# Kernel tuning notes

Hardware: AMD Instinct MI355X
Metric: run time of the kernel (lower is better)

## Reference

```python
import jax, jax.numpy as jnp
import numpy as np

N = 50000      # nodes
E = 400000     # directed edges
F_IN = 128     # input features
H0, C0 = 4, 64     # layer0: 4 heads x 64, concat -> 256
H1, C1 = 1, 256    # layer1: 1 head x 256, mean/concat -> 256
NCLS = 10
SLOPE = 0.2    # PyG GATConv leaky_relu negative_slope


def setup_inputs() -> dict:
    key = jax.random.key(0)
    ks = jax.random.split(key, 20)
    g = lambda k, shape, fan_in: jax.random.normal(k, shape, jnp.float32) * (1.0 / np.sqrt(fan_in))
    x = jax.random.normal(ks[0], (N, F_IN), jnp.float32)
    edge_index = jax.random.randint(ks[1], (2, E), 0, N)
    return {
        "x": x,
        "edge_index": edge_index,
        # GATConv layer 0: 128 -> 4 heads x 64, concat
        "W0": g(ks[2], (F_IN, H0 * C0), F_IN),
        "a_src0": g(ks[3], (H0, C0), C0),
        "a_dst0": g(ks[4], (H0, C0), C0),
        "b0": jnp.zeros((H0 * C0,), jnp.float32),
        # GATConv layer 1: 256 -> 1 head x 256, averaged
        "W1": g(ks[5], (H0 * C0, H1 * C1), H0 * C0),
        "a_src1": g(ks[6], (H1, C1), C1),
        "a_dst1": g(ks[7], (H1, C1), C1),
        "b1": jnp.zeros((C1,), jnp.float32),
        # MLP head 256 -> 512 -> 1024 -> NCLS
        "lw1": g(ks[8], (256, 512), 256), "lb1": jnp.zeros((512,), jnp.float32),
        "lw2": g(ks[9], (512, 1024), 512), "lb2": jnp.zeros((1024,), jnp.float32),
        "lw3": g(ks[10], (1024, NCLS), 1024), "lb3": jnp.zeros((NCLS,), jnp.float32),
    }


def _gat_conv(x, src, dst, valid, W, a_src, a_dst, b, heads, ch, concat):
    """PyG GATConv (eval mode, dropout=0): gather -> edge attention ->
    softmax over incoming edges per target -> scatter-sum aggregate."""
    n = x.shape[0]
    h = (x @ W).reshape(n, heads, ch)                      # [N,H,C]
    alpha_src = jnp.sum(h * a_src[None], axis=-1)          # [N,H]
    alpha_dst = jnp.sum(h * a_dst[None], axis=-1)          # [N,H]
    e = jax.nn.leaky_relu(alpha_src[src] + alpha_dst[dst], SLOPE)  # [Etot,H]
    e = jnp.where(valid[:, None], e, -1e9)                 # removed self-loops
    emax = jax.lax.stop_gradient(jax.ops.segment_max(e, dst, num_segments=n))
    w = jnp.exp(e - emax[dst]) * valid[:, None].astype(e.dtype)
    denom = jax.ops.segment_sum(w, dst, num_segments=n)    # [N,H] (>0: self-loops)
    w = w / denom[dst]
    out = jax.ops.segment_sum(h[src] * w[..., None], dst, num_segments=n)  # [N,H,C]
    out = out.reshape(n, heads * ch) if concat else out.mean(axis=1)
    return out + b


def reference(x, edge_index, W0, a_src0, a_dst0, b0, W1, a_src1, a_dst1, b1,
              lw1, lb1, lw2, lb2, lw3, lb3):
    n = x.shape[0]
    s0, d0 = edge_index[0], edge_index[1]
    loop = jnp.arange(n, dtype=s0.dtype)
    src = jnp.concatenate([s0, loop])
    dst = jnp.concatenate([d0, loop])
    valid = jnp.concatenate([s0 != d0, jnp.ones((n,), bool)])  # remove+add self-loops
    h = jax.nn.relu(_gat_conv(x, src, dst, valid, W0, a_src0, a_dst0, b0, H0, C0, True))
    h = jax.nn.relu(_gat_conv(h, src, dst, valid, W1, a_src1, a_dst1, b1, H1, C1, False))
    h = jax.nn.relu(h @ lw1 + lb1)
    h = jax.nn.relu(h @ lw2 + lb2)
    h = jax.nn.relu(h @ lw3 + lb3)
    return jax.nn.softmax(h, axis=1)
```

## Files before the change

kernel.cpp:

```cpp
#include <hip/hip_runtime.h>
#include <cstdint>
#include <cstddef>

#define F_IN   128
#define SLOPE  0.2f

typedef unsigned short u16;
typedef __attribute__((ext_vector_type(8))) short     bf16x8;
typedef __attribute__((ext_vector_type(8))) unsigned short u16x8;
typedef __attribute__((ext_vector_type(4))) unsigned short u16x4;
typedef __attribute__((ext_vector_type(4))) float     f32x4;

__device__ __forceinline__ u16 f2bf(float f) {
    unsigned u = __float_as_uint(f);
    unsigned r = u + 0x7FFFu + ((u >> 16) & 1u);
    return (u16)(r >> 16);
}
__device__ __forceinline__ float bf2f(u16 h) {
    return __uint_as_float(((unsigned)h) << 16);
}

__device__ __forceinline__ float lrelu(float v) { return v >= 0.f ? v : SLOPE * v; }

__global__ void alphas0_k(const float* __restrict__ h0, const float* __restrict__ a_src,
                          const float* __restrict__ a_dst, float* __restrict__ asrc,
                          float* __restrict__ adst, int N) {
    int gid = blockIdx.x * blockDim.x + threadIdx.x;
    int n = gid >> 6, lane = gid & 63;
    if (n >= N) return;
    #pragma unroll
    for (int h = 0; h < 4; ++h) {
        float v  = h0[(size_t)n * 256 + h * 64 + lane];
        float s1 = v * a_src[h * 64 + lane];
        float s2 = v * a_dst[h * 64 + lane];
        #pragma unroll
        for (int off = 32; off; off >>= 1) {
            s1 += __shfl_down(s1, off);
            s2 += __shfl_down(s2, off);
        }
        if (lane == 0) { asrc[n * 4 + h] = s1; adst[n * 4 + h] = s2; }
    }
}

__global__ void alphas1_k(const float* __restrict__ h1, const float* __restrict__ a_src,
                          const float* __restrict__ a_dst, float* __restrict__ asrc,
                          float* __restrict__ adst, int N) {
    int gid = blockIdx.x * blockDim.x + threadIdx.x;
    int n = gid >> 6, lane = gid & 63;
    if (n >= N) return;
    float s1 = 0.f, s2 = 0.f;
    #pragma unroll
    for (int k = 0; k < 4; ++k) {
        float v = h1[(size_t)n * 256 + k * 64 + lane];
        s1 += v * a_src[k * 64 + lane];
        s2 += v * a_dst[k * 64 + lane];
    }
    #pragma unroll
    for (int off = 32; off; off >>= 1) {
        s1 += __shfl_down(s1, off);
        s2 += __shfl_down(s2, off);
    }
    if (lane == 0) { asrc[n] = s1; adst[n] = s2; }
}

__global__ void deg_init(int* __restrict__ deg, int N) {
    int i = blockIdx.x * blockDim.x + threadIdx.x;
    if (i < N) deg[i] = 1;
}

__global__ void count_deg(const int* __restrict__ ei, int* __restrict__ deg, int E) {
    int e = blockIdx.x * blockDim.x + threadIdx.x;
    if (e >= E) return;
    int s = ei[e], d = ei[E + e];
    if (s != d) atomicAdd(&deg[d], 1);
}

__global__ void scan1(const int* __restrict__ deg, int* __restrict__ part,
                      int* __restrict__ bsum, int N) {
    __shared__ int sm[256];
    int i = blockIdx.x * 256 + threadIdx.x;
    int v = (i < N) ? deg[i] : 0;
    sm[threadIdx.x] = v; __syncthreads();
    for (int off = 1; off < 256; off <<= 1) {
        int tv = (threadIdx.x >= off) ? sm[threadIdx.x - off] : 0;
        __syncthreads();
        sm[threadIdx.x] += tv;
        __syncthreads();
    }
    if (i < N) part[i] = sm[threadIdx.x] - v;
    if (threadIdx.x == 255) bsum[blockIdx.x] = sm[255];
}

__global__ void scan2(int* __restrict__ bsum, int nb) {
    __shared__ int sm[256];
    __shared__ int carry;
    if (threadIdx.x == 0) carry = 0;
    __syncthreads();
    for (int base = 0; base < nb; base += 256) {
        int i = base + threadIdx.x;
        int v = (i < nb) ? bsum[i] : 0;
        sm[threadIdx.x] = v; __syncthreads();
        for (int off = 1; off < 256; off <<= 1) {
            int tv = (threadIdx.x >= off) ? sm[threadIdx.x - off] : 0;
            __syncthreads();
            sm[threadIdx.x] += tv;
            __syncthreads();
        }
        if (i < nb) bsum[i] = sm[threadIdx.x] - v + carry;
        __syncthreads();
        if (threadIdx.x == 0) carry += sm[255];
        __syncthreads();
    }
}

__global__ void scan3(const int* __restrict__ deg, const int* __restrict__ part,
                      const int* __restrict__ bsum, int* __restrict__ rowp,
                      int* __restrict__ cursor, int N) {
    int i = blockIdx.x * blockDim.x + threadIdx.x;
    if (i >= N) return;
    int r = part[i] + bsum[i >> 8];
    rowp[i] = r;
    cursor[i] = r;
    if (i == N - 1) rowp[N] = r + deg[i];
}

__global__ void scatter_k(const int* __restrict__ ei, int* __restrict__ cursor,
                          int* __restrict__ csr, int E, int N) {
    int e = blockIdx.x * blockDim.x + threadIdx.x;
    if (e >= E + N) return;
    int s, d;
    if (e < E) { s = ei[e]; d = ei[E + e]; if (s == d) return; }
    else       { s = d = e - E; }
    int pos = atomicAdd(&cursor[d], 1);
    csr[pos] = s;
}

__global__ void gat_gather0(const int* __restrict__ csr, const int* __restrict__ rowp,
                            const float* __restrict__ h0, const float* __restrict__ asrc,
                            const float* __restrict__ adst, const float* __restrict__ b,
                            float* __restrict__ outx, int N) {
    int gid = blockIdx.x * blockDim.x + threadIdx.x;
    int n = gid >> 6, lane = gid & 63;
    if (n >= N) return;
    int beg = rowp[n], end = rowp[n + 1];
    float4 ad = *(const float4*)(adst + (size_t)n * 4);
    float m0 = -1e30f, m1 = -1e30f, m2 = -1e30f, m3 = -1e30f;
    for (int i = beg + lane; i < end; i += 64) {
        int s = csr[i];
        float4 as = *(const float4*)(asrc + (size_t)s * 4);
        m0 = fmaxf(m0, lrelu(as.x + ad.x));
        m1 = fmaxf(m1, lrelu(as.y + ad.y));
        m2 = fmaxf(m2, lrelu(as.z + ad.z));
        m3 = fmaxf(m3, lrelu(as.w + ad.w));
    }
    #pragma unroll
    for (int off = 32; off; off >>= 1) {
        m0 = fmaxf(m0, __shfl_xor(m0, off));
        m1 = fmaxf(m1, __shfl_xor(m1, off));
        m2 = fmaxf(m2, __shfl_xor(m2, off));
        m3 = fmaxf(m3, __shfl_xor(m3, off));
    }
    float acc0 = 0.f, acc1 = 0.f, acc2 = 0.f, acc3 = 0.f;
    float den0 = 0.f, den1 = 0.f, den2 = 0.f, den3 = 0.f;
    for (int i = beg; i < end; ++i) {
        int s = csr[i];
        float4 as = *(const float4*)(asrc + (size_t)s * 4);
        float w0 = __expf(lrelu(as.x + ad.x) - m0);
        float w1 = __expf(lrelu(as.y + ad.y) - m1);
        float w2 = __expf(lrelu(as.z + ad.z) - m2);
        float w3 = __expf(lrelu(as.w + ad.w) - m3);
        den0 += w0; den1 += w1; den2 += w2; den3 += w3;
        const float* hs = h0 + (size_t)s * 256;
        acc0 += w0 * hs[lane];
        acc1 += w1 * hs[64 + lane];
        acc2 += w2 * hs[128 + lane];
        acc3 += w3 * hs[192 + lane];
    }
    float* po = outx + (size_t)n * 256;
    float v;
    v = acc0 / den0 + b[lane];       po[lane]       = v > 0.f ? v : 0.f;
    v = acc1 / den1 + b[64 + lane];  po[64 + lane]  = v > 0.f ? v : 0.f;
    v = acc2 / den2 + b[128 + lane]; po[128 + lane] = v > 0.f ? v : 0.f;
    v = acc3 / den3 + b[192 + lane]; po[192 + lane] = v > 0.f ? v : 0.f;
}

__global__ void gat_gather1(const int* __restrict__ csr, const int* __restrict__ rowp,
                            const float* __restrict__ h1, const float* __restrict__ asrc,
                            const float* __restrict__ adst, const float* __restrict__ b,
                            float* __restrict__ outx, int N) {
    int gid = blockIdx.x * blockDim.x + threadIdx.x;
    int n = gid >> 6, lane = gid & 63;
    if (n >= N) return;
    int beg = rowp[n], end = rowp[n + 1];
    float adn = adst[n];
    float mx = -1e30f;
    for (int i = beg + lane; i < end; i += 64) {
        int s = csr[i];
        mx = fmaxf(mx, lrelu(asrc[s] + adn));
    }
    #pragma unroll
    for (int off = 32; off; off >>= 1) mx = fmaxf(mx, __shfl_xor(mx, off));
    float acc0 = 0.f, acc1 = 0.f, acc2 = 0.f, acc3 = 0.f, den = 0.f;
    for (int i = beg; i < end; ++i) {
        int s = csr[i];
        float w = __expf(lrelu(asrc[s] + adn) - mx);
        den += w;
        const float* hs = h1 + (size_t)s * 256;
        acc0 += w * hs[lane];
        acc1 += w * hs[64 + lane];
        acc2 += w * hs[128 + lane];
        acc3 += w * hs[192 + lane];
    }
    float inv = 1.f / den;
    float* po = outx + (size_t)n * 256;
    float v;
    v = acc0 * inv + b[lane];       po[lane]       = v > 0.f ? v : 0.f;
    v = acc1 * inv + b[64 + lane];  po[64 + lane]  = v > 0.f ? v : 0.f;
    v = acc2 * inv + b[128 + lane]; po[128 + lane] = v > 0.f ? v : 0.f;
    v = acc3 * inv + b[192 + lane]; po[192 + lane] = v > 0.f ? v : 0.f;
}

__global__ void pack_w(const float* __restrict__ W, u16* __restrict__ out,
                       int K, int Nsrc, int NT) {
    int gid  = blockIdx.x * blockDim.x + threadIdx.x;
    int lane = gid & 63, frag = gid >> 6;
    int KT = K >> 5;
    if (frag >= KT * NT) return;
    int nt = frag % NT, kt = frag / NT;
    int n  = nt * 16 + (lane & 15);
    int k0 = kt * 32 + ((lane >> 4) << 3);
    u16x8 v8;
    #pragma unroll
    for (int i = 0; i < 8; ++i) {
        float v = (n < Nsrc) ? W[(size_t)(k0 + i) * Nsrc + n] : 0.f;
        v8[i] = f2bf(v);
    }
    *(u16x8*)(out + (size_t)(frag * 64 + lane) * 8) = v8;
}

__global__ void pack_w_hl(const float* __restrict__ W, u16* __restrict__ ohi,
                          u16* __restrict__ olo, int K, int Nsrc, int NT) {
    int gid  = blockIdx.x * blockDim.x + threadIdx.x;
    int lane = gid & 63, frag = gid >> 6;
    int KT = K >> 5;
    if (frag >= KT * NT) return;
    int nt = frag % NT, kt = frag / NT;
    int n  = nt * 16 + (lane & 15);
    int k0 = kt * 32 + ((lane >> 4) << 3);
    u16x8 h8, l8;
    #pragma unroll
    for (int i = 0; i < 8; ++i) {
        float v = (n < Nsrc) ? W[(size_t)(k0 + i) * Nsrc + n] : 0.f;
        u16 hi = f2bf(v);
        h8[i] = hi;
        l8[i] = f2bf(v - bf2f(hi));
    }
    *(u16x8*)(ohi + (size_t)(frag * 64 + lane) * 8) = h8;
    *(u16x8*)(olo + (size_t)(frag * 64 + lane) * 8) = l8;
}

__device__ __forceinline__ bf16x8 lds_afrag(const u16* buf, int Kdim, int row0, int kt, int lane) {
    int row = row0 + (lane & 15);
    int k   = kt * 32 + ((lane >> 4) << 3);
    int idx = (row * Kdim + k) ^ ((row & 7) << 3);
    return *(const bf16x8*)(buf + idx);
}

__global__ __launch_bounds__(512) void gemm_mfma(
    const float* __restrict__ A, const u16* __restrict__ bhi, const u16* __restrict__ blo,
    float* __restrict__ C, int M, int K) {
    __shared__ __align__(16) u16 Ahi[64 * 256];
    __shared__ __align__(16) u16 Alo[64 * 256];
    int t = threadIdx.x, lane = t & 63, w = t >> 6;
    int row0 = blockIdx.x * 64;
    int K4 = K >> 2;

    for (int idx = t; idx < 64 * K4; idx += 512) {
        int row = idx / K4, kq = (idx % K4) << 2;
        int gr = row0 + row;
        float4 v = make_float4(0.f, 0.f, 0.f, 0.f);
        if (gr < M) v = *(const float4*)(A + (size_t)gr * K + kq);
        u16x4 h4, l4;
        float vv[4] = {v.x, v.y, v.z, v.w};
        #pragma unroll
        for (int i = 0; i < 4; ++i) {
            u16 hi = f2bf(vv[i]);
            h4[i] = hi;
            l4[i] = f2bf(vv[i] - bf2f(hi));
        }
        int sidx = (row * K + kq) ^ ((row & 7) << 3);
        *(u16x4*)(Ahi + sidx) = h4;
        *(u16x4*)(Alo + sidx) = l4;
    }
    __syncthreads();

    int KT = K >> 5;
    f32x4 acc[4][2] = {};
    for (int kt = 0; kt < KT; ++kt) {
        bf16x8 ah[4], al[4];
        #pragma unroll
        for (int mt = 0; mt < 4; ++mt) {
            ah[mt] = lds_afrag(Ahi, K, mt * 16, kt, lane);
            al[mt] = lds_afrag(Alo, K, mt * 16, kt, lane);
        }
        #pragma unroll
        for (int nt = 0; nt < 2; ++nt) {
            int ntg = w * 2 + nt;
            size_t fo = ((size_t)(kt * 16 + ntg) * 64 + lane) * 8;
            bf16x8 bh = *(const bf16x8*)(bhi + fo);
            bf16x8 bl = *(const bf16x8*)(blo + fo);
            #pragma unroll
            for (int mt = 0; mt < 4; ++mt) {
                acc[mt][nt] = __builtin_amdgcn_mfma_f32_16x16x32_bf16(al[mt], bh, acc[mt][nt], 0, 0, 0);
                acc[mt][nt] = __builtin_amdgcn_mfma_f32_16x16x32_bf16(ah[mt], bl, acc[mt][nt], 0, 0, 0);
                acc[mt][nt] = __builtin_amdgcn_mfma_f32_16x16x32_bf16(ah[mt], bh, acc[mt][nt], 0, 0, 0);
            }
        }
    }

    #pragma unroll
    for (int mt = 0; mt < 4; ++mt)
        #pragma unroll
        for (int nt = 0; nt < 2; ++nt) {
            int col = w * 32 + nt * 16 + (lane & 15);
            #pragma unroll
            for (int j = 0; j < 4; ++j) {
                int gr = row0 + mt * 16 + ((lane >> 4) << 2) + j;
                if (gr < M) C[(size_t)gr * 256 + col] = acc[mt][nt][j];
            }
        }
}

#define NB 32

__global__ __launch_bounds__(512) void mlp_mfma(
    const float* __restrict__ m0,
    const u16* __restrict__ w1p, const float* __restrict__ lb1,
    const u16* __restrict__ w2p, const float* __restrict__ lb2,
    const u16* __restrict__ w3p, const float* __restrict__ lb3,
    float* __restrict__ out, int N) {
    __shared__ __align__(16) u16 ldsA0[32 * 256];
    __shared__ __align__(16) u16 ldsA1[32 * 512];
    __shared__ __align__(16) u16 ldsA2[32 * 1024];
    __shared__ float slog[32 * 16];

    int t = threadIdx.x, lane = t & 63, w = t >> 6;
    int nb = blockIdx.x * NB;

    slog[t] = 0.f;

    #pragma unroll
    for (int u = 0; u < 2; ++u) {
        int unit = t + u * 512;
        int row = unit >> 5, kb = (unit & 31) << 3;
        int gn = nb + row;
        u16x8 v8;
        if (gn < N) {
            const float* p = m0 + (size_t)gn * 256 + kb;
            #pragma unroll
            for (int i = 0; i < 8; ++i) v8[i] = f2bf(p[i]);
        } else {
            v8 = (u16x8)0;
        }
        int idx = (row * 256 + kb) ^ ((row & 7) << 3);
        *(u16x8*)(ldsA0 + idx) = v8;
    }
    __syncthreads();

    {
        f32x4 acc[2][4] = {};
        for (int kt = 0; kt < 8; ++kt) {
            bf16x8 a0 = lds_afrag(ldsA0, 256, 0,  kt, lane);
            bf16x8 a1 = lds_afrag(ldsA0, 256, 16, kt, lane);
            #pragma unroll
            for (int nt = 0; nt < 4; ++nt) {
                int ntg = w * 4 + nt;
                bf16x8 b = *(const bf16x8*)(w1p + ((size_t)(kt * 32 + ntg) * 64 + lane) * 8);
                acc[0][nt] = __builtin_amdgcn_mfma_f32_16x16x32_bf16(a0, b, acc[0][nt], 0, 0, 0);
                acc[1][nt] = __builtin_amdgcn_mfma_f32_16x16x32_bf16(a1, b, acc[1][nt], 0, 0, 0);
            }
        }
        #pragma unroll
        for (int mt = 0; mt < 2; ++mt)
            #pragma unroll
            for (int nt = 0; nt < 4; ++nt) {
                int col = w * 64 + nt * 16 + (lane & 15);
                float bv = lb1[col];
                #pragma unroll
                for (int j = 0; j < 4; ++j) {
                    int row = mt * 16 + ((lane >> 4) << 2) + j;
                    float v = acc[mt][nt][j] + bv;
                    v = v > 0.f ? v : 0.f;
                    ldsA1[(row * 512 + col) ^ ((row & 7) << 3)] = f2bf(v);
                }
            }
    }
    __syncthreads();

    {
        f32x4 acc[2][8] = {};
        for (int kt = 0; kt < 16; ++kt) {
            bf16x8 a0 = lds_afrag(ldsA1, 512, 0,  kt, lane);
            bf16x8 a1 = lds_afrag(ldsA1, 512, 16, kt, lane);
            #pragma unroll
            for (int nt = 0; nt < 8; ++nt) {
                int ntg = w * 8 + nt;
                bf16x8 b = *(const bf16x8*)(w2p + ((size_t)(kt * 64 + ntg) * 64 + lane) * 8);
                acc[0][nt] = __builtin_amdgcn_mfma_f32_16x16x32_bf16(a0, b, acc[0][nt], 0, 0, 0);
                acc[1][nt] = __builtin_amdgcn_mfma_f32_16x16x32_bf16(a1, b, acc[1][nt], 0, 0, 0);
            }
        }
        #pragma unroll
        for (int mt = 0; mt < 2; ++mt)
            #pragma unroll
            for (int nt = 0; nt < 8; ++nt) {
                int col = w * 128 + nt * 16 + (lane & 15);
                float bv = lb2[col];
                #pragma unroll
                for (int j = 0; j < 4; ++j) {
                    int row = mt * 16 + ((lane >> 4) << 2) + j;
                    float v = acc[mt][nt][j] + bv;
                    v = v > 0.f ? v : 0.f;
                    ldsA2[(row * 1024 + col) ^ ((row & 7) << 3)] = f2bf(v);
                }
            }
    }
    __syncthreads();

    {
        f32x4 acc[2] = {};
        #pragma unroll
        for (int kk = 0; kk < 4; ++kk) {
            int kt = w * 4 + kk;
            bf16x8 a0 = lds_afrag(ldsA2, 1024, 0,  kt, lane);
            bf16x8 a1 = lds_afrag(ldsA2, 1024, 16, kt, lane);
            bf16x8 b  = *(const bf16x8*)(w3p + ((size_t)kt * 64 + lane) * 8);
            acc[0] = __builtin_amdgcn_mfma_f32_16x16x32_bf16(a0, b, acc[0], 0, 0, 0);
            acc[1] = __builtin_amdgcn_mfma_f32_16x16x32_bf16(a1, b, acc[1], 0, 0, 0);
        }
        int col = lane & 15;
        #pragma unroll
        for (int mt = 0; mt < 2; ++mt)
            #pragma unroll
            for (int j = 0; j < 4; ++j) {
                int row = mt * 16 + ((lane >> 4) << 2) + j;
                atomicAdd(&slog[row * 16 + col], acc[mt][j]);
            }
    }
    __syncthreads();

    if (t < 32) {
        int gn = nb + t;
        if (gn < N) {
            float lg[10], m = -1e30f;
            #pragma unroll
            for (int k = 0; k < 10; ++k) {
                float v = slog[t * 16 + k] + lb3[k];
                v = v > 0.f ? v : 0.f;
                lg[k] = v;
                if (v > m) m = v;
            }
            float ssum = 0.f;
            #pragma unroll
            for (int k = 0; k < 10; ++k) { lg[k] = __expf(lg[k] - m); ssum += lg[k]; }
            float inv = 1.f / ssum;
            #pragma unroll
            for (int k = 0; k < 10; ++k) out[(size_t)gn * 10 + k] = lg[k] * inv;
        }
    }
}

extern "C" void kernel_launch(void* const* d_in, const int* in_sizes, int n_in,
                              void* d_out, int out_size, void* d_ws, size_t ws_size,
                              hipStream_t stream) {
    const float* x       = (const float*)d_in[0];
    const int*   ei      = (const int*)  d_in[1];
    const float* W0      = (const float*)d_in[2];
    const float* a_src0  = (const float*)d_in[3];
    const float* a_dst0  = (const float*)d_in[4];
    const float* b0      = (const float*)d_in[5];
    const float* W1      = (const float*)d_in[6];
    const float* a_src1  = (const float*)d_in[7];
    const float* a_dst1  = (const float*)d_in[8];
    const float* b1      = (const float*)d_in[9];
    const float* lw1     = (const float*)d_in[10];
    const float* lb1     = (const float*)d_in[11];
    const float* lw2     = (const float*)d_in[12];
    const float* lb2     = (const float*)d_in[13];
    const float* lw3     = (const float*)d_in[14];
    const float* lb3     = (const float*)d_in[15];
    float*       out     = (float*)d_out;

    const int N  = in_sizes[0] / F_IN;
    const int E  = in_sizes[1] / 2;
    const int ET = E + N;

    float* ws   = (float*)d_ws;
    size_t szH  = (size_t)N * 256;
    float* bufH = ws;
    float* bufG = ws + szH;
    float* asrc = ws + 2 * szH;
    float* adst = asrc + (size_t)N * 4;
    u16*   w1p  = (u16*)(adst + (size_t)N * 4);
    u16*   w2p  = w1p + 256 * 512;
    u16*   w3p  = w2p + 512 * 1024;
    u16*   w0h  = w3p + 1024 * 16;
    u16*   w0l  = w0h + 128 * 256;
    u16*   w1h  = w0l + 128 * 256;
    u16*   w1l  = w1h + 256 * 256;
    int*   deg  = (int*)(w1l + 256 * 256);
    int*   rowp   = deg + N;
    int*   cursor = rowp + N + 1;
    int*   part   = cursor + N;
    int*   bsum   = part + N;
    int*   csr    = bsum + 256;

    const int TB  = 256;
    const int nb1 = (N + 255) / 256;
    const int gemm_grid = (N + 63) / 64;

    pack_w<<<(8  * 32 * 64 + TB - 1) / TB, TB, 0, stream>>>(lw1, w1p, 256,  512,  32);
    pack_w<<<(16 * 64 * 64 + TB - 1) / TB, TB, 0, stream>>>(lw2, w2p, 512,  1024, 64);
    pack_w<<<(32 * 1  * 64 + TB - 1) / TB, TB, 0, stream>>>(lw3, w3p, 1024, 10,   1);
    pack_w_hl<<<(4 * 16 * 64 + TB - 1) / TB, TB, 0, stream>>>(W0, w0h, w0l, 128, 256, 16);
    pack_w_hl<<<(8 * 16 * 64 + TB - 1) / TB, TB, 0, stream>>>(W1, w1h, w1l, 256, 256, 16);

    deg_init<<<nb1, TB, 0, stream>>>(deg, N);
    count_deg<<<(E + TB - 1) / TB, TB, 0, stream>>>(ei, deg, E);
    scan1<<<nb1, TB, 0, stream>>>(deg, part, bsum, N);
    scan2<<<1, TB, 0, stream>>>(bsum, nb1);
    scan3<<<nb1, TB, 0, stream>>>(deg, part, bsum, rowp, cursor, N);
    scatter_k<<<(ET + TB - 1) / TB, TB, 0, stream>>>(ei, cursor, csr, E, N);

    gemm_mfma<<<gemm_grid, 512, 0, stream>>>(x, w0h, w0l, bufH, N, 128);
    alphas0_k<<<(N * 64 + TB - 1) / TB, TB, 0, stream>>>(bufH, a_src0, a_dst0, asrc, adst, N);
    gat_gather0<<<((size_t)N * 64 + TB - 1) / TB, TB, 0, stream>>>(csr, rowp, bufH, asrc, adst, b0, bufG, N);

    gemm_mfma<<<gemm_grid, 512, 0, stream>>>(bufG, w1h, w1l, bufH, N, 256);
    alphas1_k<<<(N * 64 + TB - 1) / TB, TB, 0, stream>>>(bufH, a_src1, a_dst1, asrc, adst, N);
    gat_gather1<<<((size_t)N * 64 + TB - 1) / TB, TB, 0, stream>>>(csr, rowp, bufH, asrc, adst, b1, bufG, N);

    mlp_mfma<<<(N + NB - 1) / NB, 512, 0, stream>>>(bufG, w1p, lb1, w2p, lb2, w3p, lb3, out, N);
}
```

Baseline: 460.1 us.

## Double MLP rows per block and stream layer-2 output through chunked layer-3

The fused MLP kernel now processes 64 nodes per block instead of 32, so each weight fragment loaded from global memory feeds twice as many MFMAs and total weight traffic across blocks is halved. To keep LDS in check, the 1024-wide second layer is computed in four 256-column chunks, and each chunk is immediately consumed by its slice of the third layer, accumulating into persistent registers. This adds two barriers per chunk, raises register pressure with 4x4 accumulators, and halves the number of blocks, which may reduce occupancy.

```diff
diff --git a/kernel.cpp b/kernel.cpp
--- a/kernel.cpp
+++ b/kernel.cpp
@@ -331,7 +331,7 @@
         }
 }
 
-#define NB 32
+#define NB 64
 
 __global__ __launch_bounds__(512) void mlp_mfma(
     const float* __restrict__ m0,
@@ -339,18 +339,19 @@
     const u16* __restrict__ w2p, const float* __restrict__ lb2,
     const u16* __restrict__ w3p, const float* __restrict__ lb3,
     float* __restrict__ out, int N) {
-    __shared__ __align__(16) u16 ldsA0[32 * 256];
-    __shared__ __align__(16) u16 ldsA1[32 * 512];
-    __shared__ __align__(16) u16 ldsA2[32 * 1024];
-    __shared__ float slog[32 * 16];
+    __shared__ __align__(16) u16 ldsA0[64 * 256];
+    __shared__ __align__(16) u16 ldsA1[64 * 512];
+    __shared__ __align__(16) u16 ldsA2[64 * 256];
+    __shared__ float slog[64 * 16];
 
     int t = threadIdx.x, lane = t & 63, w = t >> 6;
     int nb = blockIdx.x * NB;
 
     slog[t] = 0.f;
-
-    #pragma unroll
-    for (int u = 0; u < 2; ++u) {
+    slog[t + 512] = 0.f;
+
+    #pragma unroll
+    for (int u = 0; u < 4; ++u) {
         int unit = t + u * 512;
         int row = unit >> 5, kb = (unit & 31) << 3;
         int gn = nb + row;
@@ -368,20 +369,22 @@
     __syncthreads();
 
     {
-        f32x4 acc[2][4] = {};
+        f32x4 acc[4][4] = {};
         for (int kt = 0; kt < 8; ++kt) {
-            bf16x8 a0 = lds_afrag(ldsA0, 256, 0,  kt, lane);
-            bf16x8 a1 = lds_afrag(ldsA0, 256, 16, kt, lane);
+            bf16x8 a[4];
+            #pragma unroll
+            for (int mt = 0; mt < 4; ++mt) a[mt] = lds_afrag(ldsA0, 256, mt * 16, kt, lane);
             #pragma unroll
             for (int nt = 0; nt < 4; ++nt) {
                 int ntg = w * 4 + nt;
                 bf16x8 b = *(const bf16x8*)(w1p + ((size_t)(kt * 32 + ntg) * 64 + lane) * 8);
-                acc[0][nt] = __builtin_amdgcn_mfma_f32_16x16x32_bf16(a0, b, acc[0][nt], 0, 0, 0);
-                acc[1][nt] = __builtin_amdgcn_mfma_f32_16x16x32_bf16(a1, b, acc[1][nt], 0, 0, 0);
-            }
-        }
-        #pragma unroll
-        for (int mt = 0; mt < 2; ++mt)
+                #pragma unroll
+                for (int mt = 0; mt < 4; ++mt)
+                    acc[mt][nt] = __builtin_amdgcn_mfma_f32_16x16x32_bf16(a[mt], b, acc[mt][nt], 0, 0, 0);
+            }
+        }
+        #pragma unroll
+        for (int mt = 0; mt < 4; ++mt)
             #pragma unroll
             for (int nt = 0; nt < 4; ++nt) {
                 int col = w * 64 + nt * 16 + (lane & 15);
@@ -397,59 +400,61 @@
     }
     __syncthreads();
 
-    {
-        f32x4 acc[2][8] = {};
+    f32x4 acc3[4] = {};
+    for (int ch = 0; ch < 4; ++ch) {
+        f32x4 acc[4][2] = {};
         for (int kt = 0; kt < 16; ++kt) {
-            bf16x8 a0 = lds_afrag(ldsA1, 512, 0,  kt, lane);
-            bf16x8 a1 = lds_afrag(ldsA1, 512, 16, kt, lane);
-            #pragma unroll
-            for (int nt = 0; nt < 8; ++nt) {
-                int ntg = w * 8 + nt;
+            bf16x8 a[4];
+            #pragma unroll
+            for (int mt = 0; mt < 4; ++mt) a[mt] = lds_afrag(ldsA1, 512, mt * 16, kt, lane);
+            #pragma unroll
+            for (int nt = 0; nt < 2; ++nt) {
+                int ntg = ch * 16 + w * 2 + nt;
                 bf16x8 b = *(const bf16x8*)(w2p + ((size_t)(kt * 64 + ntg) * 64 + lane) * 8);
-                acc[0][nt] = __builtin_amdgcn_mfma_f32_16x16x32_bf16(a0, b, acc[0][nt], 0, 0, 0);
-                acc[1][nt] = __builtin_amdgcn_mfma_f32_16x16x32_bf16(a1, b, acc[1][nt], 0, 0, 0);
-            }
-        }
-        #pragma unroll
-        for (int mt = 0; mt < 2; ++mt)
-            #pragma unroll
-            for (int nt = 0; nt < 8; ++nt) {
-                int col = w * 128 + nt * 16 + (lane & 15);
-                float bv = lb2[col];
+                #pragma unroll
+                for (int mt = 0; mt < 4; ++mt)
+                    acc[mt][nt] = __builtin_amdgcn_mfma_f32_16x16x32_bf16(a[mt], b, acc[mt][nt], 0, 0, 0);
+            }
+        }
+        #pragma unroll
+        for (int mt = 0; mt < 4; ++mt)
+            #pragma unroll
+            for (int nt = 0; nt < 2; ++nt) {
+                int lcol = w * 32 + nt * 16 + (lane & 15);
+                float bv = lb2[ch * 256 + lcol];
                 #pragma unroll
                 for (int j = 0; j < 4; ++j) {
                     int row = mt * 16 + ((lane >> 4) << 2) + j;
                     float v = acc[mt][nt][j] + bv;
                     v = v > 0.f ? v : 0.f;
-                    ldsA2[(row * 1024 + col) ^ ((row & 7) << 3)] = f2bf(v);
+                    ldsA2[(row * 256 + lcol) ^ ((row & 7) << 3)] = f2bf(v);
                 }
             }
-    }
-    __syncthreads();
+        __syncthreads();
+        {
+            bf16x8 b3 = *(const bf16x8*)(w3p + ((size_t)(ch * 8 + w) * 64 + lane) * 8);
+            #pragma unroll
+            for (int mt = 0; mt < 4; ++mt) {
+                bf16x8 a = lds_afrag(ldsA2, 256, mt * 16, w, lane);
+                acc3[mt] = __builtin_amdgcn_mfma_f32_16x16x32_bf16(a, b3, acc3[mt], 0, 0, 0);
+            }
+        }
+        __syncthreads();
+    }
 
     {
-        f32x4 acc[2] = {};
-        #pragma unroll
-        for (int kk = 0; kk < 4; ++kk) {
-            int kt = w * 4 + kk;
-            bf16x8 a0 = lds_afrag(ldsA2, 1024, 0,  kt, lane);
-            bf16x8 a1 = lds_afrag(ldsA2, 1024, 16, kt, lane);
-            bf16x8 b  = *(const bf16x8*)(w3p + ((size_t)kt * 64 + lane) * 8);
-            acc[0] = __builtin_amdgcn_mfma_f32_16x16x32_bf16(a0, b, acc[0], 0, 0, 0);
-            acc[1] = __builtin_amdgcn_mfma_f32_16x16x32_bf16(a1, b, acc[1], 0, 0, 0);
-        }
         int col = lane & 15;
         #pragma unroll
-        for (int mt = 0; mt < 2; ++mt)
+        for (int mt = 0; mt < 4; ++mt)
             #pragma unroll
             for (int j = 0; j < 4; ++j) {
                 int row = mt * 16 + ((lane >> 4) << 2) + j;
-                atomicAdd(&slog[row * 16 + col], acc[mt][j]);
+                atomicAdd(&slog[row * 16 + col], acc3[mt][j]);
             }
     }
     __syncthreads();
 
-    if (t < 32) {
+    if (t < 64) {
         int gn = nb + t;
         if (gn < N) {
             float lg[10], m = -1e30f;
```

New measurement: 515.3 us. 1.12x slower.

## Chunk MLP layer-2 output to shrink LDS and raise occupancy in mlp_mfma

Applied to the files above, without the earlier changes.

Splits the 512->1024 MLP layer into two 512-column chunks and feeds each chunk straight into the final 1024->10 layer with a running accumulator. The 1024-wide LDS activation buffer is no longer needed, and the input buffer is aliased into a shared 512-wide buffer. LDS per block drops from about 114KB to about 66KB, and the launch bounds now request 4 waves per SIMD, so more blocks can be resident per CU. The cost is extra barriers per chunk and possible register pressure under the tighter launch bound.

```diff
diff --git a/kernel.cpp b/kernel.cpp
--- a/kernel.cpp
+++ b/kernel.cpp
@@ -333,21 +333,20 @@
 
 #define NB 32
 
-__global__ __launch_bounds__(512) void mlp_mfma(
+__global__ __launch_bounds__(512, 4) void mlp_mfma(
     const float* __restrict__ m0,
     const u16* __restrict__ w1p, const float* __restrict__ lb1,
     const u16* __restrict__ w2p, const float* __restrict__ lb2,
     const u16* __restrict__ w3p, const float* __restrict__ lb3,
     float* __restrict__ out, int N) {
-    __shared__ __align__(16) u16 ldsA0[32 * 256];
     __shared__ __align__(16) u16 ldsA1[32 * 512];
-    __shared__ __align__(16) u16 ldsA2[32 * 1024];
+    __shared__ __align__(16) u16 ldsB [32 * 512];
     __shared__ float slog[32 * 16];
 
     int t = threadIdx.x, lane = t & 63, w = t >> 6;
     int nb = blockIdx.x * NB;
 
-    slog[t] = 0.f;
+    slog[t & 511] = 0.f;
 
     #pragma unroll
     for (int u = 0; u < 2; ++u) {
@@ -363,15 +362,15 @@
             v8 = (u16x8)0;
         }
         int idx = (row * 256 + kb) ^ ((row & 7) << 3);
-        *(u16x8*)(ldsA0 + idx) = v8;
+        *(u16x8*)(ldsB + idx) = v8;
     }
     __syncthreads();
 
     {
         f32x4 acc[2][4] = {};
         for (int kt = 0; kt < 8; ++kt) {
-            bf16x8 a0 = lds_afrag(ldsA0, 256, 0,  kt, lane);
-            bf16x8 a1 = lds_afrag(ldsA0, 256, 16, kt, lane);
+            bf16x8 a0 = lds_afrag(ldsB, 256, 0,  kt, lane);
+            bf16x8 a1 = lds_afrag(ldsB, 256, 16, kt, lane);
             #pragma unroll
             for (int nt = 0; nt < 4; ++nt) {
                 int ntg = w * 4 + nt;
@@ -397,14 +396,15 @@
     }
     __syncthreads();
 
-    {
-        f32x4 acc[2][8] = {};
+    f32x4 acc3[2] = {};
+    for (int ch = 0; ch < 2; ++ch) {
+        f32x4 acc[2][4] = {};
         for (int kt = 0; kt < 16; ++kt) {
             bf16x8 a0 = lds_afrag(ldsA1, 512, 0,  kt, lane);
             bf16x8 a1 = lds_afrag(ldsA1, 512, 16, kt, lane);
             #pragma unroll
-            for (int nt = 0; nt < 8; ++nt) {
-                int ntg = w * 8 + nt;
+            for (int nt = 0; nt < 4; ++nt) {
+                int ntg = ch * 32 + w * 4 + nt;
                 bf16x8 b = *(const bf16x8*)(w2p + ((size_t)(kt * 64 + ntg) * 64 + lane) * 8);
                 acc[0][nt] = __builtin_amdgcn_mfma_f32_16x16x32_bf16(a0, b, acc[0][nt], 0, 0, 0);
                 acc[1][nt] = __builtin_amdgcn_mfma_f32_16x16x32_bf16(a1, b, acc[1][nt], 0, 0, 0);
@@ -413,38 +413,38 @@
         #pragma unroll
         for (int mt = 0; mt < 2; ++mt)
             #pragma unroll
-            for (int nt = 0; nt < 8; ++nt) {
-                int col = w * 128 + nt * 16 + (lane & 15);
-                float bv = lb2[col];
+            for (int nt = 0; nt < 4; ++nt) {
+                int lcol = w * 64 + nt * 16 + (lane & 15);
+                float bv = lb2[ch * 512 + lcol];
                 #pragma unroll
                 for (int j = 0; j < 4; ++j) {
                     int row = mt * 16 + ((lane >> 4) << 2) + j;
                     float v = acc[mt][nt][j] + bv;
                     v = v > 0.f ? v : 0.f;
-                    ldsA2[(row * 1024 + col) ^ ((row & 7) << 3)] = f2bf(v);
+                    ldsB[(row * 512 + lcol) ^ ((row & 7) << 3)] = f2bf(v);
                 }
             }
-    }
-    __syncthreads();
+        __syncthreads();
+        #pragma unroll
+        for (int q = 0; q < 2; ++q) {
+            int ktl = w * 2 + q;
+            bf16x8 b3 = *(const bf16x8*)(w3p + ((size_t)(ch * 16 + ktl) * 64 + lane) * 8);
+            bf16x8 a0 = lds_afrag(ldsB, 512, 0,  ktl, lane);
+            bf16x8 a1 = lds_afrag(ldsB, 512, 16, ktl, lane);
+            acc3[0] = __builtin_amdgcn_mfma_f32_16x16x32_bf16(a0, b3, acc3[0], 0, 0, 0);
+            acc3[1] = __builtin_amdgcn_mfma_f32_16x16x32_bf16(a1, b3, acc3[1], 0, 0, 0);
+        }
+        __syncthreads();
+    }
 
     {
-        f32x4 acc[2] = {};
-        #pragma unroll
-        for (int kk = 0; kk < 4; ++kk) {
-            int kt = w * 4 + kk;
-            bf16x8 a0 = lds_afrag(ldsA2, 1024, 0,  kt, lane);
-            bf16x8 a1 = lds_afrag(ldsA2, 1024, 16, kt, lane);
-            bf16x8 b  = *(const bf16x8*)(w3p + ((size_t)kt * 64 + lane) * 8);
-            acc[0] = __builtin_amdgcn_mfma_f32_16x16x32_bf16(a0, b, acc[0], 0, 0, 0);
-            acc[1] = __builtin_amdgcn_mfma_f32_16x16x32_bf16(a1, b, acc[1], 0, 0, 0);
-        }
         int col = lane & 15;
         #pragma unroll
         for (int mt = 0; mt < 2; ++mt)
             #pragma unroll
             for (int j = 0; j < 4; ++j) {
                 int row = mt * 16 + ((lane >> 4) << 2) + j;
-                atomicAdd(&slog[row * 16 + col], acc[mt][j]);
+                atomicAdd(&slog[row * 16 + col], acc3[mt][j]);
             }
     }
     __syncthreads();
```

New measurement: 572.3 us. 24.4% more time.
